# Performance work log

Hardware: AMD Instinct MI355X
Metric: run time of the kernel (lower is better)

The kernel has to match this reference:

```python
import jax, jax.numpy as jnp
import numpy as np

B, L, N_APPS, EMB_DIM = 4096, 1024, 10, 2


def _linear_init(key, fan_in, fan_out):
    k1, k2 = jax.random.split(key)
    s = 1.0 / np.sqrt(fan_in)
    W = jax.random.uniform(k1, (fan_in, fan_out), minval=-s, maxval=s, dtype=jnp.float32)
    b = jax.random.uniform(k2, (fan_out,), minval=-s, maxval=s, dtype=jnp.float32)
    return W, b


def setup_inputs() -> dict:
    key = jax.random.key(0)
    ks = jax.random.split(key, 12)
    # features: row 0 carries integer-valued app ids (cast with .long() in torch)
    app_row = jax.random.randint(ks[0], (B, 1, L), 0, N_APPS).astype(jnp.float32)
    loads = jax.random.normal(ks[1], (B, 2, L), dtype=jnp.float32)
    features = jnp.concatenate([app_row, loads], axis=1)  # [B,3,L]
    x_app = jax.random.randint(ks[2], (B, 1), 0, N_APPS).astype(jnp.float32)
    x_load = jax.random.normal(ks[3], (B, 2), dtype=jnp.float32)
    x_features = jnp.concatenate([x_app, x_load], axis=1)  # [B,3]
    lengths = jax.random.randint(ks[4], (B,), 1, L + 1)  # dead in the math (see notes)
    emb = jax.random.normal(ks[5], (N_APPS, EMB_DIM), dtype=jnp.float32)
    fW1, fb1 = _linear_init(ks[6], EMB_DIM + 2, 50)
    fW2, fb2 = _linear_init(ks[7], 50, 25)
    fW3, fb3 = _linear_init(ks[8], 25, 5)
    rW1, rb1 = _linear_init(ks[9], 2 * 5 + EMB_DIM + 2, 50)
    rW2, rb2 = _linear_init(ks[10], 50, 25)
    rW3, rb3 = _linear_init(ks[11], 25, 1)
    return dict(x_features=x_features, features=features, lengths=lengths, emb=emb,
                fW1=fW1, fb1=fb1, fW2=fW2, fb2=fb2, fW3=fW3, fb3=fb3,
                rW1=rW1, rb1=rb1, rW2=rW2, rb2=rb2, rW3=rW3, rb3=rb3)


def _embed(table, idx):
    # nn.Embedding(max_norm=1.0): rows are renormalized to norm <= 1 at lookup
    e = table[idx]
    n = jnp.sqrt(jnp.sum(e * e, axis=-1, keepdims=True))
    return e * jnp.minimum(1.0, 1.0 / jnp.maximum(n, 1e-7))


def _mlp3(x, W1, b1, W2, b2, W3, b3):
    h = jax.nn.relu(x @ W1 + b1)
    h = jax.nn.relu(h @ W2 + b2)
    return h @ W3 + b3


def reference(x_features, features, lengths, emb,
              fW1, fb1, fW2, fb2, fW3, fb3,
              rW1, rb1, rW2, rb2, rW3, rb3):
    # NOTE: the torch forward slices xf[:, :xl] but then overwrites it with the
    # full-length rows, so `lengths` does not affect the math. Reproduced here.
    app_ids = features[:, 0, :].astype(jnp.int32)            # [B,L]
    loads = jnp.transpose(features[:, 1:, :], (0, 2, 1))     # [B,L,2]
    e = _embed(emb, app_ids)                                  # [B,L,2]
    h = jnp.concatenate([e, loads], axis=-1)                  # [B,L,4]
    h = _mlp3(h, fW1, fb1, fW2, fb2, fW3, fb3)                # [B,L,5]
    h_sum = jnp.sum(h, axis=1)                                # [B,5]
    h_max = jnp.max(h, axis=1)                                # [B,5]
    x_app = _embed(emb, x_features[:, 0].astype(jnp.int32))   # [B,2]
    x_f = jnp.concatenate([x_app, x_features[:, 1:]], axis=-1)  # [B,4]
    hh = jnp.concatenate([h_sum, h_max, x_f], axis=-1)        # [B,14]
    return _mlp3(hh, rW1, rb1, rW2, rb2, rW3, rb3)            # [B,1]
```

## Files before the change

### kernel.cpp

```cpp
#include <hip/hip_runtime.h>
#include <stdint.h>

#define BSZ 4096
#define LSEQ 1024

typedef _Float16 half8 __attribute__((ext_vector_type(8)));
typedef __fp16 fp16x2 __attribute__((ext_vector_type(2)));
typedef float f32x4 __attribute__((ext_vector_type(4)));

union S8 { int i[4]; half8 h; int4 q; };

__device__ __forceinline__ int pack_f16(float a, float b) {
    union { _Float16 h[2]; int i; } u;
    u.h[0] = (_Float16)a;
    u.h[1] = (_Float16)b;
    return u.i;
}
__device__ __forceinline__ int relu_pkrtz(float a, float b) {
    union { fp16x2 h; int i; } u;
    u.h = __builtin_amdgcn_cvt_pkrtz(fmaxf(a, 0.f), fmaxf(b, 0.f));
    return u.i;
}
__device__ __forceinline__ void split_pair_f16(float a, float b, int& dh, int& dl) {
    _Float16 ah = (_Float16)a, bh = (_Float16)b;
    float al = a - (float)ah, bl = b - (float)bh;
    union { _Float16 h[2]; int i; } uh, ul;
    uh.h[0] = ah; uh.h[1] = bh;
    ul.h[0] = (_Float16)al; ul.h[1] = (_Float16)bl;
    dh = uh.i; dl = ul.i;
}
__device__ __forceinline__ f32x4 MFMA(half8 a, half8 b, f32x4 c) {
    return __builtin_amdgcn_mfma_f32_16x16x32_f16(a, b, c, 0, 0, 0);
}

#define WS_EMBH 5376
#define WS_EMBL 5392
#define WS_EMBR 5408

__global__ void sp_prep(const float* __restrict__ emb,
                        const float* __restrict__ fW1, const float* __restrict__ fb1,
                        const float* __restrict__ fW2, const float* __restrict__ fb2,
                        const float* __restrict__ fW3, const float* __restrict__ fb3,
                        int* __restrict__ ws)
{
    const int lane = threadIdx.x;
    const int L = lane & 15, g = lane >> 4;
    int4* wf = (int4*)ws;
    f32x4* bp = (f32x4*)ws;

    #pragma unroll
    for (int mt = 0; mt < 4; ++mt) {
        int j1 = ((mt >> 1) << 5) + ((L >> 2) << 3) + ((mt & 1) << 2) + (L & 3);
        float wv[4];
        _Float16 ah[4]; float alv[4];
        #pragma unroll
        for (int c = 0; c < 4; ++c) {
            wv[c] = (j1 < 50) ? fW1[c * 50 + j1] : 0.f;
            ah[c] = (_Float16)wv[c];
            alv[c] = wv[c] - (float)ah[c];
        }
        _Float16 v[8];
        #pragma unroll
        for (int e = 0; e < 8; ++e) {
            _Float16 x = (_Float16)0.f;
            if (g == 0) {
                if (e < 4) x = ah[e];
                else if (e < 6) x = ah[e - 4];
            } else if (g == 1) {
                if (e < 4) x = (_Float16)alv[e];
                else if (e < 6) x = (_Float16)alv[e - 4];
            }
            v[e] = x;
        }
        S8 F;
        #pragma unroll
        for (int d = 0; d < 4; ++d) {
            union { _Float16 h[2]; int i; } u;
            u.h[0] = v[2 * d]; u.h[1] = v[2 * d + 1];
            F.i[d] = u.i;
        }
        wf[mt * 64 + lane] = F.q;
    }

    #pragma unroll
    for (int kt = 0; kt < 2; ++kt) {
        #pragma unroll
        for (int mt2 = 0; mt2 < 2; ++mt2) {
            int j2 = ((L >> 2) << 3) + (mt2 << 2) + (L & 3);
            float w[8];
            #pragma unroll
            for (int r = 0; r < 8; ++r) {
                int j1v = kt * 32 + 8 * g + r;
                w[r] = (j1v < 50 && j2 < 25) ? fW2[j1v * 25 + j2] : 0.f;
            }
            S8 H, Lo;
            #pragma unroll
            for (int d = 0; d < 4; ++d) split_pair_f16(w[2*d], w[2*d+1], H.i[d], Lo.i[d]);
            wf[(4 + kt * 2 + mt2) * 64 + lane] = H.q;
            wf[(8 + kt * 2 + mt2) * 64 + lane] = Lo.q;
        }
    }

    {
        int m = L;
        float w[8];
        #pragma unroll
        for (int r = 0; r < 8; ++r) {
            int j2v = 8 * g + r;
            w[r] = (j2v < 25 && m < 5) ? fW3[j2v * 5 + m] : 0.f;
        }
        S8 H, Lo;
        #pragma unroll
        for (int d = 0; d < 4; ++d) split_pair_f16(w[2*d], w[2*d+1], H.i[d], Lo.i[d]);
        wf[12 * 64 + lane] = H.q;
        wf[13 * 64 + lane] = Lo.q;
    }

    #pragma unroll
    for (int mt = 0; mt < 4; ++mt) {
        f32x4 bv;
        #pragma unroll
        for (int r = 0; r < 4; ++r) {
            int j1 = ((mt >> 1) << 5) + 8 * g + ((mt & 1) << 2) + r;
            bv[r] = (j1 < 50) ? fb1[j1] : 0.f;
        }
        bp[(14 + mt) * 64 + lane] = bv;
    }
    #pragma unroll
    for (int mt2 = 0; mt2 < 2; ++mt2) {
        f32x4 bv;
        #pragma unroll
        for (int r = 0; r < 4; ++r) {
            int j2 = 8 * g + 4 * mt2 + r;
            bv[r] = (j2 < 25) ? fb2[j2] : 0.f;
        }
        bp[(18 + mt2) * 64 + lane] = bv;
    }
    {
        f32x4 bv;
        #pragma unroll
        for (int r = 0; r < 4; ++r) {
            int m = 4 * g + r;
            bv[r] = (m < 5) ? fb3[m] : 0.f;
        }
        bp[20 * 64 + lane] = bv;
    }

    if (lane < 10) {
        float a0 = emb[2 * lane], a1 = emb[2 * lane + 1];
        float n = sqrtf(a0 * a0 + a1 * a1);
        float s = fminf(1.f, 1.f / fmaxf(n, 1e-7f));
        float e0 = a0 * s, e1 = a1 * s;
        int dh, dl;
        split_pair_f16(e0, e1, dh, dl);
        ws[WS_EMBH + lane] = dh;
        ws[WS_EMBL + lane] = dl;
        ((float*)ws)[WS_EMBR + 2 * lane] = e0;
        ((float*)ws)[WS_EMBR + 2 * lane + 1] = e1;
    }
}

__global__ __launch_bounds__(256, 4) void sp_main(
    const float* __restrict__ x_features,
    const float* __restrict__ features,
    const int* __restrict__ ws,
    const float* __restrict__ rW1, const float* __restrict__ rb1,
    const float* __restrict__ rW2, const float* __restrict__ rb2,
    const float* __restrict__ rW3, const float* __restrict__ rb3,
    float* __restrict__ out)
{
    __shared__ int2 embhl[16];
    __shared__ float embr[20];
    __shared__ int4 bseq[LSEQ + 4];
    __shared__ float redS[4][5], redM[4][5];
    __shared__ float hhs[14];
    __shared__ float r1buf[50];

    const int t = threadIdx.x;
    const int b = blockIdx.x;
    const int lane = t & 63;
    const int wid = t >> 6;
    const int L = lane & 15;

    const int4* wf = (const int4*)ws;
    const f32x4* bp = (const f32x4*)ws;
    S8 A1[4], A2H[4], A2L[4], A3H, A3L;
    #pragma unroll
    for (int f = 0; f < 4; ++f)  A1[f].q  = wf[f * 64 + lane];
    #pragma unroll
    for (int f = 0; f < 4; ++f)  A2H[f].q = wf[(4 + f) * 64 + lane];
    #pragma unroll
    for (int f = 0; f < 4; ++f)  A2L[f].q = wf[(8 + f) * 64 + lane];
    A3H.q = wf[12 * 64 + lane];
    A3L.q = wf[13 * 64 + lane];
    f32x4 b1c[4], b2c[2], b3c;
    #pragma unroll
    for (int f = 0; f < 4; ++f) b1c[f] = bp[(14 + f) * 64 + lane];
    b2c[0] = bp[18 * 64 + lane];
    b2c[1] = bp[19 * 64 + lane];
    b3c = bp[20 * 64 + lane];

    if (t < 16) { embhl[t] = make_int2(ws[WS_EMBH + t], ws[WS_EMBL + t]); }
    if (t < 20) embr[t] = ((const float*)ws)[WS_EMBR + t];
    __syncthreads();

    const float* f0 = features + (size_t)b * (3 * LSEQ);
    {
        const float4* ra = (const float4*)(f0);
        const float4* rb = (const float4*)(f0 + LSEQ);
        const float4* rc = (const float4*)(f0 + 2 * LSEQ);
        float4 a4 = ra[t], b4 = rb[t], c4 = rc[t];
        int2 e0 = embhl[(int)a4.x];
        int2 e1 = embhl[(int)a4.y];
        int2 e2 = embhl[(int)a4.z];
        int2 e3 = embhl[(int)a4.w];
        const int base = 4 * t + (t >> 6);
        bseq[base + 0] = make_int4(e0.x, pack_f16(b4.x, c4.x), e0.y, 0);
        bseq[base + 1] = make_int4(e1.x, pack_f16(b4.y, c4.y), e1.y, 0);
        bseq[base + 2] = make_int4(e2.x, pack_f16(b4.z, c4.z), e2.y, 0);
        bseq[base + 3] = make_int4(e3.x, pack_f16(b4.w, c4.w), e3.y, 0);
    }
    __syncthreads();

    float rs[4] = {0.f, 0.f, 0.f, 0.f};
    float rm[4] = {-3.4e38f, -3.4e38f, -3.4e38f, -3.4e38f};

    const int lbase = wid * 257 + L;

    #pragma unroll 2
    for (int it = 0; it < 16; ++it) {
        S8 B1;
        B1.q = bseq[lbase + it * 16];

        f32x4 h1[4];
        #pragma unroll
        for (int mt = 0; mt < 4; ++mt)
            h1[mt] = MFMA(A1[mt].h, B1.h, b1c[mt]);

        S8 B20, B21;
        B20.i[0] = relu_pkrtz(h1[0][0], h1[0][1]);
        B20.i[1] = relu_pkrtz(h1[0][2], h1[0][3]);
        B20.i[2] = relu_pkrtz(h1[1][0], h1[1][1]);
        B20.i[3] = relu_pkrtz(h1[1][2], h1[1][3]);
        B21.i[0] = relu_pkrtz(h1[2][0], h1[2][1]);
        B21.i[1] = relu_pkrtz(h1[2][2], h1[2][3]);
        B21.i[2] = relu_pkrtz(h1[3][0], h1[3][1]);
        B21.i[3] = relu_pkrtz(h1[3][2], h1[3][3]);

        f32x4 h2[2];
        #pragma unroll
        for (int mt2 = 0; mt2 < 2; ++mt2) {
            f32x4 acc = b2c[mt2];
            acc = MFMA(A2H[mt2].h,     B20.h, acc);
            acc = MFMA(A2L[mt2].h,     B20.h, acc);
            acc = MFMA(A2H[2 + mt2].h, B21.h, acc);
            acc = MFMA(A2L[2 + mt2].h, B21.h, acc);
            h2[mt2] = acc;
        }

        S8 B3;
        B3.i[0] = relu_pkrtz(h2[0][0], h2[0][1]);
        B3.i[1] = relu_pkrtz(h2[0][2], h2[0][3]);
        B3.i[2] = relu_pkrtz(h2[1][0], h2[1][1]);
        B3.i[3] = relu_pkrtz(h2[1][2], h2[1][3]);

        f32x4 h3 = MFMA(A3H.h, B3.h, b3c);
        h3 = MFMA(A3L.h, B3.h, h3);

        #pragma unroll
        for (int r = 0; r < 4; ++r) {
            rs[r] += h3[r];
            rm[r] = fmaxf(rm[r], h3[r]);
        }
    }

    #pragma unroll
    for (int off = 1; off <= 8; off <<= 1) {
        #pragma unroll
        for (int r = 0; r < 4; ++r) {
            rs[r] += __shfl_xor(rs[r], off);
            rm[r] = fmaxf(rm[r], __shfl_xor(rm[r], off));
        }
    }
    {
        const int kg = (lane >> 4);
        if (L == 0) {
            #pragma unroll
            for (int r = 0; r < 4; ++r) {
                int m = 4 * kg + r;
                if (m < 5) { redS[wid][m] = rs[r]; redM[wid][m] = rm[r]; }
            }
        }
    }
    __syncthreads();

    if (t < 5) {
        hhs[t] = (redS[0][t] + redS[1][t]) + (redS[2][t] + redS[3][t]);
    } else if (t < 10) {
        int m = t - 5;
        hhs[t] = fmaxf(fmaxf(redM[0][m], redM[1][m]), fmaxf(redM[2][m], redM[3][m]));
    } else if (t == 10) {
        int xa = (int)x_features[b * 3];
        hhs[10] = embr[2 * xa];
        hhs[11] = embr[2 * xa + 1];
        hhs[12] = x_features[b * 3 + 1];
        hhs[13] = x_features[b * 3 + 2];
    }
    __syncthreads();

    if (t < 50) {
        float acc = rb1[t];
        #pragma unroll
        for (int i = 0; i < 14; ++i) acc += hhs[i] * rW1[i * 50 + t];
        r1buf[t] = fmaxf(acc, 0.f);
    }
    __syncthreads();

    float oacc = 0.f;
    if (t < 25) {
        float acc = rb2[t];
        #pragma unroll
        for (int k = 0; k < 50; ++k) acc += r1buf[k] * rW2[k * 25 + t];
        oacc = fmaxf(acc, 0.f) * rW3[t];
    }
    if (t < 64) {
        #pragma unroll
        for (int off = 32; off > 0; off >>= 1) oacc += __shfl_down(oacc, off);
        if (t == 0) out[b] = oacc + rb3[0];
    }
}

extern "C" void kernel_launch(void* const* d_in, const int* in_sizes, int n_in,
                              void* d_out, int out_size, void* d_ws, size_t ws_size,
                              hipStream_t stream) {
    const float* x_features = (const float*)d_in[0];
    const float* features   = (const float*)d_in[1];
    const float* emb = (const float*)d_in[3];
    const float* fW1 = (const float*)d_in[4];
    const float* fb1 = (const float*)d_in[5];
    const float* fW2 = (const float*)d_in[6];
    const float* fb2 = (const float*)d_in[7];
    const float* fW3 = (const float*)d_in[8];
    const float* fb3 = (const float*)d_in[9];
    const float* rW1 = (const float*)d_in[10];
    const float* rb1 = (const float*)d_in[11];
    const float* rW2 = (const float*)d_in[12];
    const float* rb2 = (const float*)d_in[13];
    const float* rW3 = (const float*)d_in[14];
    const float* rb3 = (const float*)d_in[15];
    float* out = (float*)d_out;
    int* ws = (int*)d_ws;

    sp_prep<<<1, 64, 0, stream>>>(emb, fW1, fb1, fW2, fb2, fW3, fb3, ws);
    sp_main<<<BSZ, 256, 0, stream>>>(x_features, features, ws,
                                     rW1, rb1, rW2, rb2, rW3, rb3, out);
}
```

Baseline: 65.60 us.

## Prefetch next B operand, pack ReLU in fp16, use scalar coalesced staging loads

```diff
diff --git a/kernel.cpp b/kernel.cpp
--- a/kernel.cpp
+++ b/kernel.cpp
@@ -17,8 +17,10 @@
     return u.i;
 }
 __device__ __forceinline__ int relu_pkrtz(float a, float b) {
-    union { fp16x2 h; int i; } u;
-    u.h = __builtin_amdgcn_cvt_pkrtz(fmaxf(a, 0.f), fmaxf(b, 0.f));
+    fp16x2 h = __builtin_amdgcn_cvt_pkrtz(a, b);
+    h = __builtin_elementwise_max(h, (fp16x2)0.f);
+    union { fp16x2 v; int i; } u;
+    u.v = h;
     return u.i;
 }
 __device__ __forceinline__ void split_pair_f16(float a, float b, int& dh, int& dl) {
@@ -205,20 +207,14 @@
     __syncthreads();
 
     const float* f0 = features + (size_t)b * (3 * LSEQ);
-    {
-        const float4* ra = (const float4*)(f0);
-        const float4* rb = (const float4*)(f0 + LSEQ);
-        const float4* rc = (const float4*)(f0 + 2 * LSEQ);
-        float4 a4 = ra[t], b4 = rb[t], c4 = rc[t];
-        int2 e0 = embhl[(int)a4.x];
-        int2 e1 = embhl[(int)a4.y];
-        int2 e2 = embhl[(int)a4.z];
-        int2 e3 = embhl[(int)a4.w];
-        const int base = 4 * t + (t >> 6);
-        bseq[base + 0] = make_int4(e0.x, pack_f16(b4.x, c4.x), e0.y, 0);
-        bseq[base + 1] = make_int4(e1.x, pack_f16(b4.y, c4.y), e1.y, 0);
-        bseq[base + 2] = make_int4(e2.x, pack_f16(b4.z, c4.z), e2.y, 0);
-        bseq[base + 3] = make_int4(e3.x, pack_f16(b4.w, c4.w), e3.y, 0);
+    #pragma unroll
+    for (int j = 0; j < 4; ++j) {
+        const int p = t + 256 * j;
+        float av = f0[p];
+        float bv = f0[LSEQ + p];
+        float cv = f0[2 * LSEQ + p];
+        int2 e = embhl[(int)av];
+        bseq[p + j] = make_int4(e.x, pack_f16(bv, cv), e.y, 0);
     }
     __syncthreads();
 
@@ -227,15 +223,18 @@
 
     const int lbase = wid * 257 + L;
 
+    S8 B1c;
+    B1c.q = bseq[lbase];
+
     #pragma unroll 2
     for (int it = 0; it < 16; ++it) {
-        S8 B1;
-        B1.q = bseq[lbase + it * 16];
+        S8 B1n;
+        B1n.q = bseq[lbase + ((it + 1) & 15) * 16];
 
         f32x4 h1[4];
         #pragma unroll
         for (int mt = 0; mt < 4; ++mt)
-            h1[mt] = MFMA(A1[mt].h, B1.h, b1c[mt]);
+            h1[mt] = MFMA(A1[mt].h, B1c.h, b1c[mt]);
 
         S8 B20, B21;
         B20.i[0] = relu_pkrtz(h1[0][0], h1[0][1]);
@@ -272,6 +271,8 @@
             rs[r] += h3[r];
             rm[r] = fmaxf(rm[r], h3[r]);
         }
+
+        B1c = B1n;
     }
 
     #pragma unroll
```

Result: faster. 55.67 us (-15.1%).
